# Kernel tuning notes

Hardware: AMD Instinct MI355X
Metric: run time of the kernel (lower is better)

Reference implementation:

```python
import jax, jax.numpy as jnp
import numpy as np

H, DK, DV, DM = 16, 64, 64, 1024
TEMP = float(np.power(DK, 0.5))
EPS = 1e-5


def setup_inputs() -> dict:
    key = jax.random.key(0)
    ks = jax.random.split(key, 12)
    B, LQ, LK = 2, 2048, 2048
    q = jax.random.normal(ks[0], (B, LQ, DM), jnp.float32)
    k = jax.random.normal(ks[1], (B, LK, DM), jnp.float32)
    v = jax.random.normal(ks[2], (B, LK, DM), jnp.float32)
    # projection weights, torch Linear convention: W [out, in], y = x @ W.T + b
    Wq = jax.random.normal(ks[3], (H * DK, DM), jnp.float32) * np.sqrt(2.0 / (DM + DK))
    Wk = jax.random.normal(ks[4], (H * DK, DM), jnp.float32) * np.sqrt(2.0 / (DM + DK))
    Wv = jax.random.normal(ks[5], (H * DV, DM), jnp.float32) * np.sqrt(2.0 / (DM + DV))
    bq = jnp.zeros((H * DK,), jnp.float32)
    bk = jnp.zeros((H * DK,), jnp.float32)
    bv = jnp.zeros((H * DV,), jnp.float32)
    Wfc = jax.random.normal(ks[6], (DM, H * DV), jnp.float32) * np.sqrt(2.0 / (DM + H * DV))
    bfc = jnp.zeros((DM,), jnp.float32)
    gamma = jnp.ones((DM,), jnp.float32)
    beta = jnp.zeros((DM,), jnp.float32)
    return {"q": q, "k": k, "v": v, "Wq": Wq, "bq": bq, "Wk": Wk, "bk": bk,
            "Wv": Wv, "bv": bv, "Wfc": Wfc, "bfc": bfc, "gamma": gamma, "beta": beta}


def reference(q, k, v, Wq, bq, Wk, bk, Wv, bv, Wfc, bfc, gamma, beta):
    B, LQ, _ = q.shape
    LK = k.shape[1]
    residual = q
    qh = (q @ Wq.T + bq).reshape(B, LQ, H, DK)   # [b, lq, h, dk]
    kh = (k @ Wk.T + bk).reshape(B, LK, H, DK)
    vh = (v @ Wv.T + bv).reshape(B, LK, H, DV)
    # scaled dot-product attention (scores laid out [h, b, lq, lk] to match (h*b) bmm)
    scores = jnp.einsum('bqhd,bkhd->hbqk', qh, kh) / TEMP
    attn = jax.nn.softmax(scores, axis=-1)
    ctx = jnp.einsum('hbqk,bkhd->bqhd', attn, vh).reshape(B, LQ, H * DV)
    out = ctx @ Wfc.T + bfc
    x = out + residual
    mean = jnp.mean(x, axis=-1, keepdims=True)
    var = jnp.var(x, axis=-1, keepdims=True)
    y = (x - mean) / jnp.sqrt(var + EPS) * gamma + beta
    attn_flat = attn.reshape(H * B, LQ, LK)
    q_flat = jnp.transpose(qh, (2, 0, 1, 3)).reshape(H * B, LQ, DK)
    return (y, attn_flat, q_flat)
```

## Files before the change

kernel.cpp:

```cpp
#include <hip/hip_runtime.h>

typedef __attribute__((ext_vector_type(8))) __bf16 bf16x8;
typedef __attribute__((ext_vector_type(4))) float f32x4;

__device__ __forceinline__ unsigned short bf16s(float f) {
    __bf16 b = (__bf16)f;
    unsigned short u;
    __builtin_memcpy(&u, &b, 2);
    return u;
}
__device__ __forceinline__ unsigned pk2(float a, float b) {
    __bf16 lo = (__bf16)a, hi = (__bf16)b;
    unsigned short ul, uh;
    __builtin_memcpy(&ul, &lo, 2);
    __builtin_memcpy(&uh, &hi, 2);
    return (unsigned)ul | ((unsigned)uh << 16);
}
#define AS1(p) ((const __attribute__((address_space(1))) void*)(p))
#define AS3(p) ((__attribute__((address_space(3))) void*)(p))

__global__ __launch_bounds__(256) void convert_kernel(
    const float* __restrict__ q, const float* __restrict__ k, const float* __restrict__ v,
    const float* __restrict__ Wq, const float* __restrict__ Wk,
    const float* __restrict__ Wv, const float* __restrict__ Wfc,
    unsigned short* __restrict__ xb, unsigned short* __restrict__ wb)
{
    size_t i = ((size_t)blockIdx.x * 256 + threadIdx.x) * 8;
    const float* src;
    unsigned short* dst;
    size_t off;
    if (i < 12582912ull) {
        int a = (int)(i >> 22);
        src = a == 0 ? q : a == 1 ? k : v;
        off = i & 4194303ull;
        dst = xb + i;
    } else {
        size_t wi = i - 12582912ull;
        int a = (int)(wi >> 20);
        src = a == 0 ? Wq : a == 1 ? Wk : a == 2 ? Wv : Wfc;
        off = wi & 1048575ull;
        dst = wb + wi;
    }
    float4 v0 = *(const float4*)(src + off);
    float4 v1 = *(const float4*)(src + off + 4);
    int4 o;
    o.x = (int)pk2(v0.x, v0.y);
    o.y = (int)pk2(v0.z, v0.w);
    o.z = (int)pk2(v1.x, v1.y);
    o.w = (int)pk2(v1.z, v1.w);
    *(int4*)dst = o;
}

__global__ __launch_bounds__(256, 3) void qkv_proj_kernel(
    const unsigned short* __restrict__ xb, const unsigned short* __restrict__ wb,
    const float* __restrict__ bq, const float* __restrict__ bk, const float* __restrict__ bv,
    unsigned short* __restrict__ qh, unsigned short* __restrict__ kh,
    unsigned short* __restrict__ vht, float* __restrict__ qflat)
{
    __shared__ unsigned short lds_a[128 * 64];
    __shared__ unsigned short lds_b[128 * 64];

    const int nb = blockIdx.x;
    const int mb = blockIdx.y;
    const int proj = nb >> 3;
    const int n0 = (nb & 7) * 128;
    const int m0 = mb * 128;

    const unsigned short* A = xb + (size_t)proj * 4194304;
    const unsigned short* B = wb + (size_t)proj * 1048576;
    const float* bias = proj == 0 ? bq : proj == 1 ? bk : bv;

    const int t = threadIdx.x, l = t & 63, w = t >> 6;
    const int wr = w >> 1, wc = w & 1;
    const int li = l & 15, g = l >> 4;
    const int sr = l >> 3;
    const int us_st = (l & 7) ^ sr;

    f32x4 acc[4][4];
    #pragma unroll
    for (int i = 0; i < 4; i++)
        #pragma unroll
        for (int j = 0; j < 4; j++) acc[i][j] = (f32x4){0.f, 0.f, 0.f, 0.f};

    for (int k0 = 0; k0 < 1024; k0 += 64) {
        __syncthreads();
        #pragma unroll
        for (int i = 0; i < 4; i++) {
            int r = i * 32 + w * 8 + sr;
            __builtin_amdgcn_global_load_lds(AS1(A + (size_t)(m0 + r) * 1024 + k0 + us_st * 8),
                                             AS3(lds_a + (i * 256 + w * 64) * 8), 16, 0, 0);
            __builtin_amdgcn_global_load_lds(AS1(B + (size_t)(n0 + r) * 1024 + k0 + us_st * 8),
                                             AS3(lds_b + (i * 256 + w * 64) * 8), 16, 0, 0);
        }
        __syncthreads();
        #pragma unroll
        for (int kk = 0; kk < 2; kk++) {
            bf16x8 af[4], bfr[4];
            int us = (kk * 4 + g) ^ (li & 7);
            #pragma unroll
            for (int mi = 0; mi < 4; mi++)
                af[mi] = *(bf16x8*)&lds_a[(wr * 64 + mi * 16 + li) * 64 + us * 8];
            #pragma unroll
            for (int ni = 0; ni < 4; ni++)
                bfr[ni] = *(bf16x8*)&lds_b[(wc * 64 + ni * 16 + li) * 64 + us * 8];
            #pragma unroll
            for (int mi = 0; mi < 4; mi++)
                #pragma unroll
                for (int ni = 0; ni < 4; ni++)
                    acc[mi][ni] = __builtin_amdgcn_mfma_f32_16x16x32_bf16(af[mi], bfr[ni], acc[mi][ni], 0, 0, 0);
        }
    }

    if (proj == 2) {
        #pragma unroll
        for (int mi = 0; mi < 4; mi++)
            #pragma unroll
            for (int ni = 0; ni < 4; ni++) {
                int c = n0 + wc * 64 + ni * 16 + li;
                float bl = bias[c];
                int hh = c >> 6, dd = c & 63;
                int row0 = m0 + wr * 64 + mi * 16 + g * 4;
                int bb = row0 >> 11, kk2 = row0 & 2047;
                unsigned lo = pk2(acc[mi][ni][0] + bl, acc[mi][ni][1] + bl);
                unsigned hi = pk2(acc[mi][ni][2] + bl, acc[mi][ni][3] + bl);
                int2 u; u.x = (int)lo; u.y = (int)hi;
                *(int2*)(vht + ((size_t)((bb * 16 + hh) * 64 + dd)) * 2048 + kk2) = u;
            }
    } else {
        unsigned short* OUT = proj == 0 ? qh : kh;
        const float osc = proj == 0 ? 0.125f : 1.0f;
        #pragma unroll
        for (int mi = 0; mi < 4; mi++)
            #pragma unroll
            for (int ni = 0; ni < 4; ni++) {
                int c = n0 + wc * 64 + ni * 16 + li;
                float bl = bias[c];
                int hh = c >> 6, dd = c & 63;
                int row0 = m0 + wr * 64 + mi * 16 + g * 4;
                #pragma unroll
                for (int j = 0; j < 4; j++) {
                    int row = row0 + j;
                    float val = acc[mi][ni][j] + bl;
                    OUT[(size_t)row * 1024 + c] = bf16s(val * osc);
                    if (proj == 0) {
                        int bb = row >> 11, lq = row & 2047;
                        __builtin_nontemporal_store(val,
                            qflat + (((size_t)(hh * 2 + bb)) * 2048 + lq) * 64 + dd);
                    }
                }
            }
    }
}

__global__ __launch_bounds__(512, 4) void attn_kernel(
    const unsigned short* __restrict__ qh, const unsigned short* __restrict__ kh,
    const unsigned short* __restrict__ vht, float* __restrict__ attn_out,
    unsigned short* __restrict__ ctx)
{
    __shared__ unsigned short lds_k[2][8192];
    __shared__ unsigned short lds_vt[2][8192];
    __shared__ unsigned short lds_p[8192];

    const int qt = blockIdx.x, hb = blockIdx.y;
    const int h = hb >> 1, b_ = hb & 1;
    const int q0 = qt * 128;
    const int t = threadIdx.x, l = t & 63, w = t >> 6;
    const int li = l & 15, g = l >> 4;

    const unsigned short* Qb = qh + (size_t)(b_ * 2048 + q0) * 1024 + h * 64;
    const unsigned short* Kb = kh + (size_t)(b_ * 2048) * 1024 + h * 64;
    const unsigned short* VTb = vht + (size_t)(b_ * 16 + h) * 131072;
    float* Ab = attn_out + ((size_t)hb * 2048 + q0) * 2048;

    bf16x8 aq[2];
    #pragma unroll
    for (int kk = 0; kk < 2; kk++)
        aq[kk] = *(const bf16x8*)(Qb + (size_t)(w * 16 + li) * 1024 + kk * 32 + g * 8);

    const int sr8 = l >> 3;
    const int us8 = (l & 7) ^ sr8;

#define STAGE_K(KT, BUF) do { \
    _Pragma("unroll") \
    for (int c = 0; c < 2; c++) { \
        int r_ = w * 16 + c * 8 + sr8; \
        __builtin_amdgcn_global_load_lds(AS1(Kb + (size_t)((KT) * 128 + r_) * 1024 + us8 * 8), \
            AS3(lds_k[BUF] + w * 1024 + c * 512), 16, 0, 0); \
    } } while (0)

#define QKT(BUF, S) do { \
    _Pragma("unroll") \
    for (int ni = 0; ni < 8; ni++) (S)[ni] = (f32x4){0.f, 0.f, 0.f, 0.f}; \
    __builtin_amdgcn_s_setprio(1); \
    _Pragma("unroll") \
    for (int kk = 0; kk < 2; kk++) { \
        int us = ((kk * 4 + g) ^ (li & 7)) * 8; \
        _Pragma("unroll") \
        for (int ni = 0; ni < 8; ni++) { \
            bf16x8 bk = *(bf16x8*)&lds_k[BUF][(ni * 16 + li) * 64 + us]; \
            (S)[ni] = __builtin_amdgcn_mfma_f32_16x16x32_bf16(bk, aq[kk], (S)[ni], 0, 0, 0); \
        } \
    } \
    __builtin_amdgcn_s_setprio(0); \
    } while (0)

    float ssum = 0.f;
    STAGE_K(0, 0);
    __syncthreads();
    for (int kt = 0; kt < 16; kt++) {
        const int cur = kt & 1;
        if (kt < 15) STAGE_K(kt + 1, cur ^ 1);
        f32x4 s[8];
        QKT(cur, s);
        float ps = 0.f;
        #pragma unroll
        for (int ni = 0; ni < 8; ni++)
            #pragma unroll
            for (int j = 0; j < 4; j++) ps += __expf(s[ni][j]);
        ssum += ps;
        __syncthreads();
    }
    ssum += __shfl_xor(ssum, 16, 64);
    ssum += __shfl_xor(ssum, 32, 64);
    const float rl = 1.f / ssum;

    f32x4 cacc[4];
    #pragma unroll
    for (int ni = 0; ni < 4; ni++) cacc[ni] = (f32x4){0.f, 0.f, 0.f, 0.f};

    const int vd0 = w * 4 + g;
    const int vd1 = vd0 + 32;
    const int vsl0 = (li ^ (vd0 & 15)) * 8;
    const int vsl1 = (li ^ (vd1 & 15)) * 8;

    STAGE_K(0, 0);
    {
        int4 va = *(const int4*)(VTb + (size_t)vd0 * 2048 + li * 8);
        int4 vb = *(const int4*)(VTb + (size_t)vd1 * 2048 + li * 8);
        *(int4*)&lds_vt[0][vd0 * 128 + vsl0] = va;
        *(int4*)&lds_vt[0][vd1 * 128 + vsl1] = vb;
    }
    __syncthreads();

    f32x4 s[8];
    for (int kt = 0; kt < 16; kt++) {
        const int cur = kt & 1;
        if (kt > 0) {
            #pragma unroll
            for (int ni = 0; ni < 8; ni++)
                __builtin_nontemporal_store(s[ni],
                    (f32x4*)(Ab + (size_t)(w * 16 + li) * 2048 + (kt - 1) * 128 + ni * 16 + 4 * g));
        }
        int4 va, vb;
        if (kt < 15) {
            STAGE_K(kt + 1, cur ^ 1);
            va = *(const int4*)(VTb + (size_t)vd0 * 2048 + (kt + 1) * 128 + li * 8);
            vb = *(const int4*)(VTb + (size_t)vd1 * 2048 + (kt + 1) * 128 + li * 8);
        }
        QKT(cur, s);
        #pragma unroll
        for (int half = 0; half < 2; half++) {
            #pragma unroll
            for (int ni4 = 0; ni4 < 4; ni4++) {
                int ni = half * 4 + ni4;
                float p0 = __expf(s[ni][0]) * rl;
                float p1 = __expf(s[ni][1]) * rl;
                float p2 = __expf(s[ni][2]) * rl;
                float p3 = __expf(s[ni][3]) * rl;
                s[ni] = (f32x4){p0, p1, p2, p3};
                int chunk = (2 * ni4 + (g >> 1)) ^ (li & 7);
                int base = (w * 16 + li) * 64 + chunk * 8 + 4 * (g & 1);
                *(unsigned*)&lds_p[base]     = pk2(p0, p1);
                *(unsigned*)&lds_p[base + 2] = pk2(p2, p3);
            }
            __builtin_amdgcn_s_setprio(1);
            #pragma unroll
            for (int ks = 0; ks < 2; ks++) {
                int us = ((ks * 4 + g) ^ (li & 7)) * 8;
                bf16x8 ap = *(bf16x8*)&lds_p[(w * 16 + li) * 64 + us];
                int vus = (((half * 2 + ks) * 4 + g) ^ li) * 8;
                #pragma unroll
                for (int ni = 0; ni < 4; ni++) {
                    bf16x8 bv2 = *(bf16x8*)&lds_vt[cur][(ni * 16 + li) * 128 + vus];
                    cacc[ni] = __builtin_amdgcn_mfma_f32_16x16x32_bf16(ap, bv2, cacc[ni], 0, 0, 0);
                }
            }
            __builtin_amdgcn_s_setprio(0);
        }
        if (kt < 15) {
            *(int4*)&lds_vt[cur ^ 1][vd0 * 128 + vsl0] = va;
            *(int4*)&lds_vt[cur ^ 1][vd1 * 128 + vsl1] = vb;
        }
        __syncthreads();
    }
    #pragma unroll
    for (int ni = 0; ni < 8; ni++)
        __builtin_nontemporal_store(s[ni],
            (f32x4*)(Ab + (size_t)(w * 16 + li) * 2048 + 15 * 128 + ni * 16 + 4 * g));
#undef STAGE_K
#undef QKT

    #pragma unroll
    for (int ni = 0; ni < 4; ni++)
        #pragma unroll
        for (int j = 0; j < 4; j++) {
            int r = w * 16 + g * 4 + j;
            int d = ni * 16 + li;
            ctx[(size_t)(b_ * 2048 + q0 + r) * 1024 + h * 64 + d] = bf16s(cacc[ni][j]);
        }
}

__global__ __launch_bounds__(256, 3) void fc_kernel(
    const unsigned short* __restrict__ ctx, const unsigned short* __restrict__ wfcb,
    const float* __restrict__ bfc, const float* __restrict__ resid,
    float* __restrict__ xout)
{
    __shared__ unsigned short lds_a[128 * 64];
    __shared__ unsigned short lds_b[128 * 64];

    const int n0 = blockIdx.x * 128;
    const int m0 = blockIdx.y * 128;
    const int t = threadIdx.x, l = t & 63, w = t >> 6;
    const int wr = w >> 1, wc = w & 1;
    const int li = l & 15, g = l >> 4;
    const int sr = l >> 3;
    const int us_st = (l & 7) ^ sr;

    f32x4 acc[4][4];
    #pragma unroll
    for (int i = 0; i < 4; i++)
        #pragma unroll
        for (int j = 0; j < 4; j++) acc[i][j] = (f32x4){0.f, 0.f, 0.f, 0.f};

    for (int k0 = 0; k0 < 1024; k0 += 64) {
        __syncthreads();
        #pragma unroll
        for (int i = 0; i < 4; i++) {
            int r = i * 32 + w * 8 + sr;
            __builtin_amdgcn_global_load_lds(AS1(ctx + (size_t)(m0 + r) * 1024 + k0 + us_st * 8),
                                             AS3(lds_a + (i * 256 + w * 64) * 8), 16, 0, 0);
            __builtin_amdgcn_global_load_lds(AS1(wfcb + (size_t)(n0 + r) * 1024 + k0 + us_st * 8),
                                             AS3(lds_b + (i * 256 + w * 64) * 8), 16, 0, 0);
        }
        __syncthreads();
        #pragma unroll
        for (int kk = 0; kk < 2; kk++) {
            bf16x8 af[4], bfr[4];
            int us = (kk * 4 + g) ^ (li & 7);
            #pragma unroll
            for (int mi = 0; mi < 4; mi++)
                af[mi] = *(bf16x8*)&lds_a[(wr * 64 + mi * 16 + li) * 64 + us * 8];
            #pragma unroll
            for (int ni = 0; ni < 4; ni++)
                bfr[ni] = *(bf16x8*)&lds_b[(wc * 64 + ni * 16 + li) * 64 + us * 8];
            #pragma unroll
            for (int mi = 0; mi < 4; mi++)
                #pragma unroll
                for (int ni = 0; ni < 4; ni++)
                    acc[mi][ni] = __builtin_amdgcn_mfma_f32_16x16x32_bf16(af[mi], bfr[ni], acc[mi][ni], 0, 0, 0);
        }
    }

    #pragma unroll
    for (int mi = 0; mi < 4; mi++)
        #pragma unroll
        for (int ni = 0; ni < 4; ni++) {
            int col = n0 + wc * 64 + ni * 16 + li;
            float bl = bfc[col];
            #pragma unroll
            for (int j = 0; j < 4; j++) {
                int row = m0 + wr * 64 + mi * 16 + g * 4 + j;
                float val = acc[mi][ni][j] + bl + resid[(size_t)row * 1024 + col];
                xout[(size_t)row * 1024 + col] = val;
            }
        }
}

__global__ __launch_bounds__(256) void ln_kernel(
    float* __restrict__ x, const float* __restrict__ gamma,
    const float* __restrict__ beta)
{
    __shared__ float red[2][4];
    const int row = blockIdx.x;
    const int t = threadIdx.x;
    float4 v = *(const float4*)(x + (size_t)row * 1024 + t * 4);
    float s = v.x + v.y + v.z + v.w;
    float ss = v.x * v.x + v.y * v.y + v.z * v.z + v.w * v.w;
    #pragma unroll
    for (int msk = 1; msk < 64; msk <<= 1) {
        s += __shfl_xor(s, msk, 64);
        ss += __shfl_xor(ss, msk, 64);
    }
    int w = t >> 6, l = t & 63;
    if (l == 0) { red[0][w] = s; red[1][w] = ss; }
    __syncthreads();
    s = red[0][0] + red[0][1] + red[0][2] + red[0][3];
    ss = red[1][0] + red[1][1] + red[1][2] + red[1][3];
    float mean = s * (1.f / 1024.f);
    float var = ss * (1.f / 1024.f) - mean * mean;
    float rstd = rsqrtf(var + 1e-5f);
    float4 g4 = *(const float4*)(gamma + t * 4);
    float4 b4 = *(const float4*)(beta + t * 4);
    float4 o;
    o.x = (v.x - mean) * rstd * g4.x + b4.x;
    o.y = (v.y - mean) * rstd * g4.y + b4.y;
    o.z = (v.z - mean) * rstd * g4.z + b4.z;
    o.w = (v.w - mean) * rstd * g4.w + b4.w;
    *(float4*)(x + (size_t)row * 1024 + t * 4) = o;
}

extern "C" void kernel_launch(void* const* d_in, const int* in_sizes, int n_in,
                              void* d_out, int out_size, void* d_ws, size_t ws_size,
                              hipStream_t stream)
{
    const float* q     = (const float*)d_in[0];
    const float* k     = (const float*)d_in[1];
    const float* v     = (const float*)d_in[2];
    const float* Wq    = (const float*)d_in[3];
    const float* bq    = (const float*)d_in[4];
    const float* Wk    = (const float*)d_in[5];
    const float* bk    = (const float*)d_in[6];
    const float* Wv    = (const float*)d_in[7];
    const float* bv    = (const float*)d_in[8];
    const float* Wfc   = (const float*)d_in[9];
    const float* bfc   = (const float*)d_in[10];
    const float* gamma = (const float*)d_in[11];
    const float* beta  = (const float*)d_in[12];

    float* y     = (float*)d_out;
    float* attn  = (float*)d_out + 4194304;
    float* qflat = (float*)d_out + 4194304 + 134217728;

    unsigned short* xb = (unsigned short*)attn;

    char* ws = (char*)d_ws;
    unsigned short* qh  = (unsigned short*)(ws);
    unsigned short* kh  = (unsigned short*)(ws + 8388608ull);
    unsigned short* vht = (unsigned short*)(ws + 16777216ull);
    unsigned short* ctx = (unsigned short*)(ws + 25165824ull);
    unsigned short* wb  = (unsigned short*)(ws + 33554432ull);

    convert_kernel<<<8192, 256, 0, stream>>>(q, k, v, Wq, Wk, Wv, Wfc, xb, wb);
    qkv_proj_kernel<<<dim3(24, 32), 256, 0, stream>>>(xb, wb, bq, bk, bv, qh, kh, vht, qflat);
    attn_kernel<<<dim3(16, 32), 512, 0, stream>>>(qh, kh, vht, attn, ctx);
    fc_kernel<<<dim3(8, 32), 256, 0, stream>>>(ctx, wb + 3145728, bfc, q, y);
    ln_kernel<<<4096, 256, 0, stream>>>(y, gamma, beta);
}
```

Before: 286.2 us.

## Read K fragments directly from global memory in softmax-denominator pass

The first pass over K, which only accumulates the softmax row sums, no longer stages K tiles through double-buffered LDS with barriers. Each wave now loads its bf16 K fragments straight from global memory (relying on L2/L1 reuse across waves) and runs the MFMAs without any __syncthreads. The P-tile store to LDS is also merged from two 32-bit writes into one 64-bit write. This removes barrier and LDS-copy overhead but adds redundant global loads across waves and may expose memory latency.

```diff
diff --git a/kernel.cpp b/kernel.cpp
--- a/kernel.cpp
+++ b/kernel.cpp
@@ -205,20 +205,38 @@
     } while (0)
 
     float ssum = 0.f;
-    STAGE_K(0, 0);
-    __syncthreads();
-    for (int kt = 0; kt < 16; kt++) {
-        const int cur = kt & 1;
-        if (kt < 15) STAGE_K(kt + 1, cur ^ 1);
-        f32x4 s[8];
-        QKT(cur, s);
-        float ps = 0.f;
-        #pragma unroll
-        for (int ni = 0; ni < 8; ni++)
-            #pragma unroll
-            for (int j = 0; j < 4; j++) ps += __expf(s[ni][j]);
-        ssum += ps;
-        __syncthreads();
+    {
+        const unsigned short* Kl = Kb + (size_t)li * 1024 + g * 8;
+        for (int kt = 0; kt < 16; kt++) {
+            const unsigned short* Kt = Kl + (size_t)kt * 131072;
+            f32x4 s[8];
+            #pragma unroll
+            for (int ni = 0; ni < 8; ni++) s[ni] = (f32x4){0.f, 0.f, 0.f, 0.f};
+            #pragma unroll
+            for (int hf = 0; hf < 2; hf++) {
+                bf16x8 f0[4], f1[4];
+                #pragma unroll
+                for (int n4 = 0; n4 < 4; n4++) {
+                    int ni = hf * 4 + n4;
+                    f0[n4] = *(const bf16x8*)(Kt + ni * 16384);
+                    f1[n4] = *(const bf16x8*)(Kt + ni * 16384 + 32);
+                }
+                __builtin_amdgcn_s_setprio(1);
+                #pragma unroll
+                for (int n4 = 0; n4 < 4; n4++) {
+                    int ni = hf * 4 + n4;
+                    s[ni] = __builtin_amdgcn_mfma_f32_16x16x32_bf16(f0[n4], aq[0], s[ni], 0, 0, 0);
+                    s[ni] = __builtin_amdgcn_mfma_f32_16x16x32_bf16(f1[n4], aq[1], s[ni], 0, 0, 0);
+                }
+                __builtin_amdgcn_s_setprio(0);
+            }
+            float ps = 0.f;
+            #pragma unroll
+            for (int ni = 0; ni < 8; ni++)
+                #pragma unroll
+                for (int j = 0; j < 4; j++) ps += __expf(s[ni][j]);
+            ssum += ps;
+        }
     }
     ssum += __shfl_xor(ssum, 16, 64);
     ssum += __shfl_xor(ssum, 32, 64);
@@ -270,8 +288,8 @@
                 s[ni] = (f32x4){p0, p1, p2, p3};
                 int chunk = (2 * ni4 + (g >> 1)) ^ (li & 7);
                 int base = (w * 16 + li) * 64 + chunk * 8 + 4 * (g & 1);
-                *(unsigned*)&lds_p[base]     = pk2(p0, p1);
-                *(unsigned*)&lds_p[base + 2] = pk2(p2, p3);
+                int2 pw; pw.x = (int)pk2(p0, p1); pw.y = (int)pk2(p2, p3);
+                *(int2*)&lds_p[base] = pw;
             }
             __builtin_amdgcn_s_setprio(1);
             #pragma unroll
```

After: 310.0 us. 8.3% more time.
